# Kernel tuning notes

Hardware: AMD Instinct MI355X
Metric: run time of the kernel (lower is better)

The kernel has to match this reference:

```python
import jax, jax.numpy as jnp
import numpy as np

N_NODES = 50000
N_EDGES = 800000
D = 64


def setup_inputs() -> dict:
    key = jax.random.key(0)
    k1, k2, k3, k4, k5 = jax.random.split(key, 5)
    graph_embedding = jax.random.normal(k1, (N_NODES, D), dtype=jnp.float32)
    weight = jax.random.normal(k2, (1, D), dtype=jnp.float32)  # xavier-like scale not critical
    src = jax.random.randint(k3, (N_EDGES,), 0, N_NODES, dtype=jnp.int32)
    dst = jax.random.randint(k4, (N_EDGES,), 0, N_NODES, dtype=jnp.int32)
    e_feat = jax.random.randint(k5, (N_EDGES,), 0, 6, dtype=jnp.int32)
    return {"graph_embedding": graph_embedding, "weight": weight,
            "src": src, "dst": dst, "e_feat": e_feat}


def reference(graph_embedding, weight, src, dst, e_feat):
    n_nodes = graph_embedding.shape[0]
    # emb == ft == ft0 == ft3 == ft4 == ft5 in the original module
    emb = jax.nn.elu(graph_embedding * weight)  # [N, D]
    e = e_feat  # integer edge-type codes; original float cast + == gives same result
    # two-hop message: ft + [e==0]*ft0 + [e==4]*ft4 + [e==5]*ft5, all equal to emb[src]
    scale = (1.0 + (e == 0).astype(emb.dtype)
                 + (e == 4).astype(emb.dtype)
                 + (e == 5).astype(emb.dtype))  # [E]
    msg2 = emb[src] * scale[:, None]  # [E, D]
    ft_twohop = jax.ops.segment_sum(msg2, dst, num_segments=n_nodes)  # [N, D]
    # one-hop message: select two-hop feature of source on edges of type 3
    msg1 = jnp.where((e == 3)[:, None], ft_twohop[src], jnp.zeros((), emb.dtype))  # [E, D]
    res = jax.ops.segment_sum(msg1, dst, num_segments=n_nodes)  # [N, D]
    return res
```

## Files before the change

kernel.cpp:

```cpp
#include <hip/hip_runtime.h>

#define D 64
#define CAP 48
#define CAP3 16
#define NBW 256
#define QW 64
#define EPB 2048
#define CELL 40
#define SEGSTRIDE 4608

__device__ __forceinline__ unsigned short f2bf(float f) {
    union { float f; unsigned u; } v; v.f = f;
    unsigned r = (v.u + 0x7FFFu + ((v.u >> 16) & 1u)) >> 16;
    return (unsigned short)r;
}
__device__ __forceinline__ float bflo(unsigned u) {
    union { unsigned x; float f; } v; v.x = u << 16; return v.f;
}
__device__ __forceinline__ float bfhi(unsigned u) {
    union { unsigned x; float f; } v; v.x = u & 0xFFFF0000u; return v.f;
}

__global__ __launch_bounds__(256) void k_combo(
        const int* __restrict__ src, const int* __restrict__ dst, const int* __restrict__ ef,
        unsigned* __restrict__ seg, int* __restrict__ segcnt,
        const float4* __restrict__ g4, const float4* __restrict__ w4,
        unsigned short* __restrict__ embb,
        int n_edges, int nb, int nblkA, int n_elems) {
    __shared__ unsigned lcell[256 * CELL];
    __shared__ int lcnt[256];
    int tid = threadIdx.x;

    if (blockIdx.x < (unsigned)nblkA) {
        int base = blockIdx.x * EPB;
        lcnt[tid] = 0;
        __syncthreads();

        int e0 = base + tid * 8;
        if (e0 + 8 <= n_edges) {
            int4 d0 = *(const int4*)(dst + e0), d1 = *(const int4*)(dst + e0 + 4);
            int4 s0 = *(const int4*)(src + e0), s1 = *(const int4*)(src + e0 + 4);
            int4 f0 = *(const int4*)(ef  + e0), f1 = *(const int4*)(ef  + e0 + 4);
            int ds[8] = {d0.x, d0.y, d0.z, d0.w, d1.x, d1.y, d1.z, d1.w};
            int ss[8] = {s0.x, s0.y, s0.z, s0.w, s1.x, s1.y, s1.z, s1.w};
            int fs[8] = {f0.x, f0.y, f0.z, f0.w, f1.x, f1.y, f1.z, f1.w};
            #pragma unroll
            for (int j = 0; j < 8; ++j) {
                int b = ds[j] >> 8;
                unsigned rec = (unsigned)ss[j] | ((unsigned)fs[j] << 16)
                             | ((unsigned)(ds[j] & 255) << 19);
                int pos = atomicAdd(&lcnt[b], 1);
                if (pos < CELL) lcell[b * CELL + pos] = rec;
            }
        } else {
            for (int j = 0; j < 8; ++j) {
                int e = e0 + j;
                if (e < n_edges) {
                    int d = dst[e];
                    unsigned rec = (unsigned)src[e] | ((unsigned)ef[e] << 16)
                                 | ((unsigned)(d & 255) << 19);
                    int pos = atomicAdd(&lcnt[d >> 8], 1);
                    if (pos < CELL) lcell[(d >> 8) * CELL + pos] = rec;
                }
            }
        }
        __syncthreads();

        if (tid < nb) {
            int v = lcnt[tid]; if (v > CELL) v = CELL;
            if (v > 0) {
                int off = atomicAdd(&segcnt[tid], v);
                unsigned* dstp = seg + (size_t)tid * SEGSTRIDE + off;
                for (int k = 0; k < v; ++k) dstp[k] = lcell[tid * CELL + k];
            }
        }
    } else {
        int i = (blockIdx.x - nblkA) * 256 + tid;
        if (i * 8 >= n_elems) return;
        float4 a = g4[i * 2];
        float4 b = g4[i * 2 + 1];
        float4 wa = w4[(i * 2) & 15];
        float4 wb = w4[(i * 2 + 1) & 15];
        a.x *= wa.x; a.y *= wa.y; a.z *= wa.z; a.w *= wa.w;
        b.x *= wb.x; b.y *= wb.y; b.z *= wb.z; b.w *= wb.w;
        a.x = a.x > 0.f ? a.x : (expf(a.x) - 1.f);
        a.y = a.y > 0.f ? a.y : (expf(a.y) - 1.f);
        a.z = a.z > 0.f ? a.z : (expf(a.z) - 1.f);
        a.w = a.w > 0.f ? a.w : (expf(a.w) - 1.f);
        b.x = b.x > 0.f ? b.x : (expf(b.x) - 1.f);
        b.y = b.y > 0.f ? b.y : (expf(b.y) - 1.f);
        b.z = b.z > 0.f ? b.z : (expf(b.z) - 1.f);
        b.w = b.w > 0.f ? b.w : (expf(b.w) - 1.f);
        uint4 o;
        o.x = (unsigned)f2bf(a.x) | ((unsigned)f2bf(a.y) << 16);
        o.y = (unsigned)f2bf(a.z) | ((unsigned)f2bf(a.w) << 16);
        o.z = (unsigned)f2bf(b.x) | ((unsigned)f2bf(b.y) << 16);
        o.w = (unsigned)f2bf(b.z) | ((unsigned)f2bf(b.w) << 16);
        *(uint4*)(embb + (size_t)i * 8) = o;
    }
}

__global__ __launch_bounds__(512) void k_fuse(
        const unsigned short* __restrict__ embb,
        const unsigned* __restrict__ seg, const int* __restrict__ segcnt,
        unsigned short* __restrict__ ftb, int* __restrict__ cnt3, unsigned* __restrict__ ell3,
        int nb, int n_nodes) {
    __shared__ unsigned lpay[QW * CAP];
    __shared__ unsigned lpay3[QW * CAP3];
    __shared__ int lc[QW];
    __shared__ int lc3[QW];
    int bucket = blockIdx.x >> 2;
    int q      = blockIdx.x & 3;
    int lo     = bucket * NBW + q * QW;
    int tid = threadIdx.x;
    int wave = tid >> 6, lane = tid & 63;
    for (int i = tid; i < QW; i += 512) { lc[i] = 0; lc3[i] = 0; }
    __syncthreads();

    int total = segcnt[bucket];
    if (total > SEGSTRIDE) total = SEGSTRIDE;
    const unsigned* segp = seg + (size_t)bucket * SEGSTRIDE;
    int total4 = total & ~3;
    for (int i = tid * 4; i < total4; i += 512 * 4) {
        uint4 rv = *(const uint4*)(segp + i);
        unsigned rs[4] = {rv.x, rv.y, rv.z, rv.w};
        #pragma unroll
        for (int k = 0; k < 4; ++k) {
            unsigned rec = rs[k];
            unsigned r = rec >> 19;
            if ((int)(r >> 6) == q) {
                unsigned rr = r & 63;
                unsigned pl = rec & 0x7FFFFu;
                int pos = atomicAdd(&lc[rr], 1);
                if (pos < CAP) lpay[rr * CAP + pos] = pl;
                if (((rec >> 16) & 7u) == 3u) {
                    int p3 = atomicAdd(&lc3[rr], 1);
                    if (p3 < CAP3) lpay3[rr * CAP3 + p3] = pl;
                }
            }
        }
    }
    if (tid < (total - total4)) {
        unsigned rec = segp[total4 + tid];
        unsigned r = rec >> 19;
        if ((int)(r >> 6) == q) {
            unsigned rr = r & 63;
            unsigned pl = rec & 0x7FFFFu;
            int pos = atomicAdd(&lc[rr], 1);
            if (pos < CAP) lpay[rr * CAP + pos] = pl;
            if (((rec >> 16) & 7u) == 3u) {
                int p3 = atomicAdd(&lc3[rr], 1);
                if (p3 < CAP3) lpay3[rr * CAP3 + p3] = pl;
            }
        }
    }
    __syncthreads();

    int grp = lane >> 3;
    int sub = lane & 7;
    int dq8 = sub * 8;
    #pragma unroll 2
    for (int n = wave; n < QW; n += 8) {
        int node = lo + n;
        if (node >= n_nodes) break;
        int deg = lc[n]; deg = deg < CAP ? deg : CAP;
        const unsigned* row = lpay + n * CAP;
        float acc0 = 0.f, acc1 = 0.f, acc2 = 0.f, acc3 = 0.f;
        float acc4 = 0.f, acc5 = 0.f, acc6 = 0.f, acc7 = 0.f;
        for (int base = 0; base < deg; base += 16) {
            int e0 = base + grp, e1 = e0 + 8;
            int i0 = 0, i1 = 0;
            float s0 = 0.f, s1 = 0.f;
            if (e0 < deg) { unsigned p = row[e0]; i0 = p & 0xFFFF; int et = p >> 16;
                            s0 = 1.f + (float)(et == 0) + (float)(et == 4) + (float)(et == 5); }
            if (e1 < deg) { unsigned p = row[e1]; i1 = p & 0xFFFF; int et = p >> 16;
                            s1 = 1.f + (float)(et == 0) + (float)(et == 4) + (float)(et == 5); }
            uint4 u0 = *(const uint4*)(embb + (size_t)i0 * D + dq8);
            uint4 u1 = *(const uint4*)(embb + (size_t)i1 * D + dq8);
            acc0 += bflo(u0.x) * s0 + bflo(u1.x) * s1;
            acc1 += bfhi(u0.x) * s0 + bfhi(u1.x) * s1;
            acc2 += bflo(u0.y) * s0 + bflo(u1.y) * s1;
            acc3 += bfhi(u0.y) * s0 + bfhi(u1.y) * s1;
            acc4 += bflo(u0.z) * s0 + bflo(u1.z) * s1;
            acc5 += bfhi(u0.z) * s0 + bfhi(u1.z) * s1;
            acc6 += bflo(u0.w) * s0 + bflo(u1.w) * s1;
            acc7 += bfhi(u0.w) * s0 + bfhi(u1.w) * s1;
        }
        #pragma unroll
        for (int m = 8; m <= 32; m <<= 1) {
            acc0 += __shfl_xor(acc0, m); acc1 += __shfl_xor(acc1, m);
            acc2 += __shfl_xor(acc2, m); acc3 += __shfl_xor(acc3, m);
            acc4 += __shfl_xor(acc4, m); acc5 += __shfl_xor(acc5, m);
            acc6 += __shfl_xor(acc6, m); acc7 += __shfl_xor(acc7, m);
        }
        if (grp == 0) {
            uint4 o;
            o.x = (unsigned)f2bf(acc0) | ((unsigned)f2bf(acc1) << 16);
            o.y = (unsigned)f2bf(acc2) | ((unsigned)f2bf(acc3) << 16);
            o.z = (unsigned)f2bf(acc4) | ((unsigned)f2bf(acc5) << 16);
            o.w = (unsigned)f2bf(acc6) | ((unsigned)f2bf(acc7) << 16);
            *(uint4*)(ftb + (size_t)node * D + dq8) = o;
        }
        if (lane < CAP3) ell3[(size_t)node * CAP3 + lane] = lpay3[n * CAP3 + lane];
        if (lane == 0) cnt3[node] = lc3[n] < CAP3 ? lc3[n] : CAP3;
    }
}

__global__ void k_onehop_gather(const unsigned short* __restrict__ ftb,
                                const int* __restrict__ cnt3,
                                const unsigned* __restrict__ ell3,
                                float* __restrict__ out, int n_nodes) {
    int gid  = blockIdx.x * blockDim.x + threadIdx.x;
    int node = gid >> 6;
    int lane = gid & 63;
    if (node >= n_nodes) return;
    int deg = cnt3[node];
    const unsigned* row = ell3 + (size_t)node * CAP3;
    int grp = lane >> 3;
    int sub = lane & 7;
    int dq8 = sub * 8;
    int e0 = grp, e1 = grp + 8;
    int i0 = 0, i1 = 0;
    float s0 = 0.f, s1 = 0.f;
    if (e0 < deg) { i0 = row[e0] & 0xFFFF; s0 = 1.f; }
    if (e1 < deg) { i1 = row[e1] & 0xFFFF; s1 = 1.f; }
    uint4 u0 = *(const uint4*)(ftb + (size_t)i0 * D + dq8);
    uint4 u1 = *(const uint4*)(ftb + (size_t)i1 * D + dq8);
    float acc0 = bflo(u0.x) * s0 + bflo(u1.x) * s1;
    float acc1 = bfhi(u0.x) * s0 + bfhi(u1.x) * s1;
    float acc2 = bflo(u0.y) * s0 + bflo(u1.y) * s1;
    float acc3 = bfhi(u0.y) * s0 + bfhi(u1.y) * s1;
    float acc4 = bflo(u0.z) * s0 + bflo(u1.z) * s1;
    float acc5 = bfhi(u0.z) * s0 + bfhi(u1.z) * s1;
    float acc6 = bflo(u0.w) * s0 + bflo(u1.w) * s1;
    float acc7 = bfhi(u0.w) * s0 + bfhi(u1.w) * s1;
    #pragma unroll
    for (int m = 8; m <= 32; m <<= 1) {
        acc0 += __shfl_xor(acc0, m); acc1 += __shfl_xor(acc1, m);
        acc2 += __shfl_xor(acc2, m); acc3 += __shfl_xor(acc3, m);
        acc4 += __shfl_xor(acc4, m); acc5 += __shfl_xor(acc5, m);
        acc6 += __shfl_xor(acc6, m); acc7 += __shfl_xor(acc7, m);
    }
    if (grp == 0) {
        float4 oa = {acc0, acc1, acc2, acc3};
        float4 ob = {acc4, acc5, acc6, acc7};
        *(float4*)(out + (size_t)node * D + dq8)     = oa;
        *(float4*)(out + (size_t)node * D + dq8 + 4) = ob;
    }
}

extern "C" void kernel_launch(void* const* d_in, const int* in_sizes, int n_in,
                              void* d_out, int out_size, void* d_ws, size_t ws_size,
                              hipStream_t stream) {
    const float* g   = (const float*)d_in[0];
    const float* w   = (const float*)d_in[1];
    const int*   src = (const int*)d_in[2];
    const int*   dst = (const int*)d_in[3];
    const int*   ef  = (const int*)d_in[4];
    float* out = (float*)d_out;

    int n_elems = in_sizes[0];
    int n_nodes = n_elems / D;
    int n_edges = in_sizes[2];
    int nblkA   = (n_edges + EPB - 1) / EPB;
    int nb      = (n_nodes + NBW - 1) / NBW;

    unsigned short* embb   = (unsigned short*)d_ws;
    unsigned short* ftb    = embb + n_elems;
    int*            cnt3   = (int*)(ftb + n_elems);
    int*            segcnt = cnt3 + n_nodes + 64;
    unsigned*       ell3   = (unsigned*)(segcnt + nb + 64);
    unsigned*       seg    = ell3 + (size_t)n_nodes * CAP3;

    hipMemsetAsync(segcnt, 0, (size_t)nb * sizeof(int), stream);

    {
        int embBlocks = (n_elems / 8 + 255) / 256;
        k_combo<<<nblkA + embBlocks, 256, 0, stream>>>(
            src, dst, ef, seg, segcnt,
            (const float4*)g, (const float4*)w, embb,
            n_edges, nb, nblkA, n_elems);
    }
    k_fuse<<<nb * 4, 512, 0, stream>>>(embb, seg, segcnt, ftb, cnt3, ell3,
                                       nb, n_nodes);
    {
        long long total = (long long)n_nodes * D;
        int blocks = (int)((total + 255) / 256);
        k_onehop_gather<<<blocks, 256, 0, stream>>>(ftb, cnt3, ell3, out, n_nodes);
    }
}
```

Baseline: 129.9 us.

## Bin edges by source tile and accumulate two-hop sums with LDS atomics

```diff
diff --git a/kernel.cpp b/kernel.cpp
--- a/kernel.cpp
+++ b/kernel.cpp
@@ -1,13 +1,17 @@
 #include <hip/hip_runtime.h>
 
 #define D 64
-#define CAP 48
 #define CAP3 16
 #define NBW 256
 #define QW 64
 #define EPB 2048
-#define CELL 40
-#define SEGSTRIDE 4608
+#define TILES 4
+#define NBUCK 196
+#define NBINS (NBUCK * TILES)
+#define BCELL 16
+#define SEGS 1536
+#define MQCAP 768
+#define FSTRIDE 65
 
 __device__ __forceinline__ unsigned short f2bf(float f) {
     union { float f; unsigned u; } v; v.f = f;
@@ -26,14 +30,14 @@
         unsigned* __restrict__ seg, int* __restrict__ segcnt,
         const float4* __restrict__ g4, const float4* __restrict__ w4,
         unsigned short* __restrict__ embb,
-        int n_edges, int nb, int nblkA, int n_elems) {
-    __shared__ unsigned lcell[256 * CELL];
-    __shared__ int lcnt[256];
+        int n_edges, int nblkA, int n_elems) {
+    __shared__ unsigned lcell[NBINS * BCELL];
+    __shared__ int lcnt[NBINS];
     int tid = threadIdx.x;
 
     if (blockIdx.x < (unsigned)nblkA) {
         int base = blockIdx.x * EPB;
-        lcnt[tid] = 0;
+        for (int i = tid; i < NBINS; i += 256) lcnt[i] = 0;
         __syncthreads();
 
         int e0 = base + tid * 8;
@@ -46,32 +50,34 @@
             int fs[8] = {f0.x, f0.y, f0.z, f0.w, f1.x, f1.y, f1.z, f1.w};
             #pragma unroll
             for (int j = 0; j < 8; ++j) {
-                int b = ds[j] >> 8;
+                int b = (ds[j] >> 8) * TILES + (ss[j] >> 14);
                 unsigned rec = (unsigned)ss[j] | ((unsigned)fs[j] << 16)
                              | ((unsigned)(ds[j] & 255) << 19);
                 int pos = atomicAdd(&lcnt[b], 1);
-                if (pos < CELL) lcell[b * CELL + pos] = rec;
+                if (pos < BCELL) lcell[b * BCELL + pos] = rec;
             }
         } else {
             for (int j = 0; j < 8; ++j) {
                 int e = e0 + j;
                 if (e < n_edges) {
-                    int d = dst[e];
-                    unsigned rec = (unsigned)src[e] | ((unsigned)ef[e] << 16)
+                    int d = dst[e], s = src[e];
+                    int b = (d >> 8) * TILES + (s >> 14);
+                    unsigned rec = (unsigned)s | ((unsigned)ef[e] << 16)
                                  | ((unsigned)(d & 255) << 19);
-                    int pos = atomicAdd(&lcnt[d >> 8], 1);
-                    if (pos < CELL) lcell[(d >> 8) * CELL + pos] = rec;
+                    int pos = atomicAdd(&lcnt[b], 1);
+                    if (pos < BCELL) lcell[b * BCELL + pos] = rec;
                 }
             }
         }
         __syncthreads();
 
-        if (tid < nb) {
-            int v = lcnt[tid]; if (v > CELL) v = CELL;
+        for (int b = tid; b < NBINS; b += 256) {
+            int v = lcnt[b]; if (v > BCELL) v = BCELL;
             if (v > 0) {
-                int off = atomicAdd(&segcnt[tid], v);
-                unsigned* dstp = seg + (size_t)tid * SEGSTRIDE + off;
-                for (int k = 0; k < v; ++k) dstp[k] = lcell[tid * CELL + k];
+                int off = atomicAdd(&segcnt[b], v);
+                if (off + v > SEGS) v = (SEGS > off) ? (SEGS - off) : 0;
+                unsigned* dstp = seg + (size_t)b * SEGS + off;
+                for (int k = 0; k < v; ++k) dstp[k] = lcell[b * BCELL + k];
             }
         }
     } else {
@@ -104,105 +110,89 @@
         const unsigned short* __restrict__ embb,
         const unsigned* __restrict__ seg, const int* __restrict__ segcnt,
         unsigned short* __restrict__ ftb, int* __restrict__ cnt3, unsigned* __restrict__ ell3,
-        int nb, int n_nodes) {
-    __shared__ unsigned lpay[QW * CAP];
+        int n_nodes) {
+    __shared__ float facc[QW * FSTRIDE];
     __shared__ unsigned lpay3[QW * CAP3];
-    __shared__ int lc[QW];
     __shared__ int lc3[QW];
+    __shared__ unsigned mq[MQCAP];
+    __shared__ int mqc;
     int bucket = blockIdx.x >> 2;
     int q      = blockIdx.x & 3;
     int lo     = bucket * NBW + q * QW;
-    int tid = threadIdx.x;
+    int tid  = threadIdx.x;
     int wave = tid >> 6, lane = tid & 63;
-    for (int i = tid; i < QW; i += 512) { lc[i] = 0; lc3[i] = 0; }
-    __syncthreads();
-
-    int total = segcnt[bucket];
-    if (total > SEGSTRIDE) total = SEGSTRIDE;
-    const unsigned* segp = seg + (size_t)bucket * SEGSTRIDE;
-    int total4 = total & ~3;
-    for (int i = tid * 4; i < total4; i += 512 * 4) {
-        uint4 rv = *(const uint4*)(segp + i);
-        unsigned rs[4] = {rv.x, rv.y, rv.z, rv.w};
-        #pragma unroll
-        for (int k = 0; k < 4; ++k) {
-            unsigned rec = rs[k];
+    int grp = lane >> 3, sub = lane & 7;
+
+    for (int i = tid; i < QW * FSTRIDE; i += 512) facc[i] = 0.f;
+    for (int i = tid; i < QW; i += 512) lc3[i] = 0;
+
+    for (int t = 0; t < TILES; ++t) {
+        __syncthreads();
+        if (tid == 0) mqc = 0;
+        __syncthreads();
+        int bin = bucket * TILES + t;
+        int cnt = segcnt[bin]; if (cnt > SEGS) cnt = SEGS;
+        const unsigned* sp = seg + (size_t)bin * SEGS;
+        for (int i = tid; i < cnt; i += 512) {
+            unsigned rec = sp[i];
             unsigned r = rec >> 19;
             if ((int)(r >> 6) == q) {
-                unsigned rr = r & 63;
-                unsigned pl = rec & 0x7FFFFu;
-                int pos = atomicAdd(&lc[rr], 1);
-                if (pos < CAP) lpay[rr * CAP + pos] = pl;
+                int pos = atomicAdd(&mqc, 1);
+                if (pos < MQCAP) mq[pos] = rec;
                 if (((rec >> 16) & 7u) == 3u) {
+                    unsigned rr = r & 63u;
                     int p3 = atomicAdd(&lc3[rr], 1);
-                    if (p3 < CAP3) lpay3[rr * CAP3 + p3] = pl;
+                    if (p3 < CAP3) lpay3[rr * CAP3 + p3] = rec & 0xFFFFu;
                 }
             }
         }
-    }
-    if (tid < (total - total4)) {
-        unsigned rec = segp[total4 + tid];
-        unsigned r = rec >> 19;
-        if ((int)(r >> 6) == q) {
-            unsigned rr = r & 63;
-            unsigned pl = rec & 0x7FFFFu;
-            int pos = atomicAdd(&lc[rr], 1);
-            if (pos < CAP) lpay[rr * CAP + pos] = pl;
-            if (((rec >> 16) & 7u) == 3u) {
-                int p3 = atomicAdd(&lc3[rr], 1);
-                if (p3 < CAP3) lpay3[rr * CAP3 + p3] = pl;
+        __syncthreads();
+        int m = mqc; if (m > MQCAP) m = MQCAP;
+        #pragma unroll 2
+        for (int j = wave * 8; j < m; j += 64) {
+            int idx = j + grp;
+            if (idx < m) {
+                unsigned rec = mq[idx];
+                unsigned rr = (rec >> 19) & 63u;
+                int s  = rec & 0xFFFF;
+                int et = (rec >> 16) & 7;
+                float sc = (et == 0 || et == 4 || et == 5) ? 2.f : 1.f;
+                uint4 u = *(const uint4*)(embb + (size_t)s * D + sub * 8);
+                float* fp = facc + rr * FSTRIDE + sub * 8;
+                atomicAdd(fp + 0, bflo(u.x) * sc);
+                atomicAdd(fp + 1, bfhi(u.x) * sc);
+                atomicAdd(fp + 2, bflo(u.y) * sc);
+                atomicAdd(fp + 3, bfhi(u.y) * sc);
+                atomicAdd(fp + 4, bflo(u.z) * sc);
+                atomicAdd(fp + 5, bfhi(u.z) * sc);
+                atomicAdd(fp + 6, bflo(u.w) * sc);
+                atomicAdd(fp + 7, bfhi(u.w) * sc);
             }
         }
     }
     __syncthreads();
 
-    int grp = lane >> 3;
-    int sub = lane & 7;
-    int dq8 = sub * 8;
-    #pragma unroll 2
-    for (int n = wave; n < QW; n += 8) {
+    {
+        int n  = tid >> 3;
+        int dd = (tid & 7) * 8;
         int node = lo + n;
-        if (node >= n_nodes) break;
-        int deg = lc[n]; deg = deg < CAP ? deg : CAP;
-        const unsigned* row = lpay + n * CAP;
-        float acc0 = 0.f, acc1 = 0.f, acc2 = 0.f, acc3 = 0.f;
-        float acc4 = 0.f, acc5 = 0.f, acc6 = 0.f, acc7 = 0.f;
-        for (int base = 0; base < deg; base += 16) {
-            int e0 = base + grp, e1 = e0 + 8;
-            int i0 = 0, i1 = 0;
-            float s0 = 0.f, s1 = 0.f;
-            if (e0 < deg) { unsigned p = row[e0]; i0 = p & 0xFFFF; int et = p >> 16;
-                            s0 = 1.f + (float)(et == 0) + (float)(et == 4) + (float)(et == 5); }
-            if (e1 < deg) { unsigned p = row[e1]; i1 = p & 0xFFFF; int et = p >> 16;
-                            s1 = 1.f + (float)(et == 0) + (float)(et == 4) + (float)(et == 5); }
-            uint4 u0 = *(const uint4*)(embb + (size_t)i0 * D + dq8);
-            uint4 u1 = *(const uint4*)(embb + (size_t)i1 * D + dq8);
-            acc0 += bflo(u0.x) * s0 + bflo(u1.x) * s1;
-            acc1 += bfhi(u0.x) * s0 + bfhi(u1.x) * s1;
-            acc2 += bflo(u0.y) * s0 + bflo(u1.y) * s1;
-            acc3 += bfhi(u0.y) * s0 + bfhi(u1.y) * s1;
-            acc4 += bflo(u0.z) * s0 + bflo(u1.z) * s1;
-            acc5 += bfhi(u0.z) * s0 + bfhi(u1.z) * s1;
-            acc6 += bflo(u0.w) * s0 + bflo(u1.w) * s1;
-            acc7 += bfhi(u0.w) * s0 + bfhi(u1.w) * s1;
-        }
-        #pragma unroll
-        for (int m = 8; m <= 32; m <<= 1) {
-            acc0 += __shfl_xor(acc0, m); acc1 += __shfl_xor(acc1, m);
-            acc2 += __shfl_xor(acc2, m); acc3 += __shfl_xor(acc3, m);
-            acc4 += __shfl_xor(acc4, m); acc5 += __shfl_xor(acc5, m);
-            acc6 += __shfl_xor(acc6, m); acc7 += __shfl_xor(acc7, m);
-        }
-        if (grp == 0) {
+        if (node < n_nodes) {
+            const float* fp = facc + n * FSTRIDE + dd;
             uint4 o;
-            o.x = (unsigned)f2bf(acc0) | ((unsigned)f2bf(acc1) << 16);
-            o.y = (unsigned)f2bf(acc2) | ((unsigned)f2bf(acc3) << 16);
-            o.z = (unsigned)f2bf(acc4) | ((unsigned)f2bf(acc5) << 16);
-            o.w = (unsigned)f2bf(acc6) | ((unsigned)f2bf(acc7) << 16);
-            *(uint4*)(ftb + (size_t)node * D + dq8) = o;
-        }
-        if (lane < CAP3) ell3[(size_t)node * CAP3 + lane] = lpay3[n * CAP3 + lane];
-        if (lane == 0) cnt3[node] = lc3[n] < CAP3 ? lc3[n] : CAP3;
+            o.x = (unsigned)f2bf(fp[0]) | ((unsigned)f2bf(fp[1]) << 16);
+            o.y = (unsigned)f2bf(fp[2]) | ((unsigned)f2bf(fp[3]) << 16);
+            o.z = (unsigned)f2bf(fp[4]) | ((unsigned)f2bf(fp[5]) << 16);
+            o.w = (unsigned)f2bf(fp[6]) | ((unsigned)f2bf(fp[7]) << 16);
+            *(uint4*)(ftb + (size_t)node * D + dd) = o;
+        }
+    }
+    for (int i = tid; i < QW; i += 512) {
+        int node = lo + i;
+        if (node < n_nodes) cnt3[node] = lc3[i] < CAP3 ? lc3[i] : CAP3;
+    }
+    for (int i = tid; i < QW * CAP3; i += 512) {
+        int node = lo + (i >> 4);
+        if (node < n_nodes) ell3[(size_t)node * CAP3 + (i & 15)] = lpay3[i];
     }
 }
 
@@ -264,25 +254,25 @@
     int n_edges = in_sizes[2];
     int nblkA   = (n_edges + EPB - 1) / EPB;
     int nb      = (n_nodes + NBW - 1) / NBW;
+    int npad    = nb * NBW;
 
     unsigned short* embb   = (unsigned short*)d_ws;
     unsigned short* ftb    = embb + n_elems;
     int*            cnt3   = (int*)(ftb + n_elems);
-    int*            segcnt = cnt3 + n_nodes + 64;
-    unsigned*       ell3   = (unsigned*)(segcnt + nb + 64);
-    unsigned*       seg    = ell3 + (size_t)n_nodes * CAP3;
-
-    hipMemsetAsync(segcnt, 0, (size_t)nb * sizeof(int), stream);
+    int*            segcnt = cnt3 + npad;
+    unsigned*       ell3   = (unsigned*)(segcnt + NBINS + 64);
+    unsigned*       seg    = ell3 + (size_t)npad * CAP3;
+
+    hipMemsetAsync(segcnt, 0, (size_t)NBINS * sizeof(int), stream);
 
     {
         int embBlocks = (n_elems / 8 + 255) / 256;
         k_combo<<<nblkA + embBlocks, 256, 0, stream>>>(
             src, dst, ef, seg, segcnt,
             (const float4*)g, (const float4*)w, embb,
-            n_edges, nb, nblkA, n_elems);
-    }
-    k_fuse<<<nb * 4, 512, 0, stream>>>(embb, seg, segcnt, ftb, cnt3, ell3,
-                                       nb, n_nodes);
+            n_edges, nblkA, n_elems);
+    }
+    k_fuse<<<nb * 4, 512, 0, stream>>>(embb, seg, segcnt, ftb, cnt3, ell3, n_nodes);
     {
         long long total = (long long)n_nodes * D;
         int blocks = (int)((total + 255) / 256);
```

New measurement: 453.5 us. +249.2%, slower.
